# Kernel optimization log

Measured on AMD Instinct MI355X. Metric: run time of the kernel, lower is better.

Reference implementation:

```python
import jax, jax.numpy as jnp
import numpy as np
from jax import lax

N_WAY, N_SUPPORT, N_QUERY = 16, 256, 512
D_IN, D_EMB = 4096, 1024
N_CLUSTERS, MAX_ITER = 5, 100


def setup_inputs() -> dict:
    key = jax.random.key(0)
    k1, k2, kw, kb = jax.random.split(key, 4)
    support = jax.random.normal(k1, (N_WAY, N_SUPPORT, D_IN), jnp.float32)
    query = jax.random.normal(k2, (N_WAY, N_QUERY, D_IN), jnp.float32)
    W = jax.random.normal(kw, (D_IN, D_EMB), jnp.float32) / np.float32(np.sqrt(D_IN))
    b = jax.random.normal(kb, (D_EMB,), jnp.float32) * 0.01
    return {"support": support, "query": query, "W": W, "b": b}


def _sqdist(x, c):
    # x [n,d], c [k,d] -> [n,k] squared euclidean distances
    return (jnp.sum(x * x, -1, keepdims=True)
            - 2.0 * (x @ c.T)
            + jnp.sum(c * c, -1))


def _kmeans(x, init):
    # x [n,d], init [k,d]; fixed-iteration Lloyd's kmeans (converged state is a
    # fixed point of the update, matching the torch early-break semantics).
    n = x.shape[0]
    ones = jnp.ones((n,), x.dtype)

    def step(c, _):
        assign = jnp.argmin(_sqdist(x, c), axis=1)              # [n]
        sums = jax.ops.segment_sum(x, assign, num_segments=N_CLUSTERS)
        cnt = jax.ops.segment_sum(ones, assign, num_segments=N_CLUSTERS)
        # empty cluster keeps its old centroid
        new_c = jnp.where(cnt[:, None] > 0,
                          sums / jnp.maximum(cnt, 1.0)[:, None], c)
        return new_c, None

    c, _ = lax.scan(step, init, None, length=MAX_ITER)
    return c


def _forward(support, query, W, b):
    # encoder: shared linear over flattened (n_way * n) rows
    s = (support.reshape(-1, D_IN) @ W + b).reshape(N_WAY, N_SUPPORT, D_EMB)
    q = (query.reshape(-1, D_IN) @ W + b).reshape(N_WAY, N_QUERY, D_EMB)

    # per-class kmeans init: random subset of that class's support embeddings
    keys = jax.random.split(jax.random.key(42), N_WAY)

    def init_fn(key, class_emb):
        idx = jax.random.permutation(key, N_SUPPORT)[:N_CLUSTERS]
        return class_emb[idx]

    inits = jax.vmap(init_fn)(keys, s)                 # [n_way, k, d]
    cluster_protos = jax.vmap(_kmeans)(s, inits)       # [n_way, k, d]
    class_protos = cluster_protos.mean(axis=1)         # [n_way, d]

    # cdist(query_emb [b,n,d], protos [c,d]) -> [b,n,c]
    d2 = (jnp.sum(q * q, -1)[..., None]
          - 2.0 * jnp.einsum('bnd,cd->bnc', q, class_protos)
          + jnp.sum(class_protos * class_protos, -1))
    distances = jnp.sqrt(jnp.maximum(d2, 0.0))
    return -distances                                  # logits [n_way, n_query, n_classes]


def reference(support, query, W, b):
    return _forward(support, query, W, b)
```

## Files before the change

kernel.cpp:

```cpp
#include <hip/hip_runtime.h>
#include <cstdint>
#include <cstddef>


typedef __attribute__((ext_vector_type(4))) float f32x4;
typedef __attribute__((ext_vector_type(8))) short s16x8;
typedef __attribute__((ext_vector_type(4))) short s16x4;
typedef __attribute__((ext_vector_type(8))) __bf16 bf16x8;

__device__ __forceinline__ unsigned short f2bf(float f) {
  unsigned u = __float_as_uint(f);
  return (unsigned short)((u + 0x7FFFu + ((u >> 16) & 1u)) >> 16);
}
__device__ __forceinline__ float bf2f(unsigned short h) {
  return __uint_as_float(((unsigned)h) << 16);
}

typedef const __attribute__((address_space(1))) void GV;
typedef __attribute__((address_space(3))) void LV;
__device__ __forceinline__ void gload_lds16(const void* g, void* l) {
  __builtin_amdgcn_global_load_lds((GV*)g, (LV*)l, 16, 0, 0);
}
__device__ __forceinline__ f32x4 mfma16(bf16x8 a, bf16x8 b, f32x4 c) {
  return __builtin_amdgcn_mfma_f32_16x16x32_bf16(a, b, c, 0, 0, 0);
}
__device__ __forceinline__ float wave_sum(float v) {
#pragma unroll
  for (int st = 1; st < 64; st <<= 1) v += __shfl_xor(v, st);
  return v;
}

__device__ __forceinline__ void tf2x32(unsigned k0, unsigned k1, unsigned x0,
                                       unsigned x1, unsigned& y0, unsigned& y1) {
  unsigned ks0 = k0, ks1 = k1, ks2 = k0 ^ k1 ^ 0x1BD11BDAu;
  x0 += ks0; x1 += ks1;
  const int rA[4] = {13, 15, 26, 6};
  const int rB[4] = {17, 29, 16, 24};
#define ROTL(v, d) (((v) << (d)) | ((v) >> (32 - (d))))
#define RG(R)                                     \
  _Pragma("unroll") for (int i = 0; i < 4; i++) { \
    x0 += x1; x1 = ROTL(x1, R[i]); x1 ^= x0;      \
  }
  RG(rA); x0 += ks1; x1 += ks2 + 1u;
  RG(rB); x0 += ks2; x1 += ks0 + 2u;
  RG(rA); x0 += ks0; x1 += ks1 + 3u;
  RG(rB); x0 += ks1; x1 += ks2 + 4u;
  RG(rA); x0 += ks2; x1 += ks0 + 5u;
#undef RG
#undef ROTL
  y0 = x0; y1 = x1;
}

__global__ __launch_bounds__(256) void prep_sw_k(
    const float* __restrict__ W, const float* __restrict__ sup,
    short* __restrict__ WhiT, short* __restrict__ WloT,
    short* __restrict__ Shi, short* __restrict__ Slo) {
  __shared__ float tile[64][65];
  int t = threadIdx.x;
  if (blockIdx.x < 1024) {
    int bk = blockIdx.x & 63, bn = blockIdx.x >> 6;
#pragma unroll
    for (int i = 0; i < 4; i++) {
      int row = i * 16 + (t >> 4);
      int col = (t & 15) * 4;
      f32x4 v =
          *(const f32x4*)(W + (size_t)(bk * 64 + row) * 1024 + bn * 64 + col);
      tile[row][col + 0] = v[0]; tile[row][col + 1] = v[1];
      tile[row][col + 2] = v[2]; tile[row][col + 3] = v[3];
    }
    __syncthreads();
#pragma unroll
    for (int i = 0; i < 4; i++) {
      int nrow = i * 16 + (t >> 4);
      int kcol = (t & 15) * 4;
      s16x4 hv, lv;
#pragma unroll
      for (int e = 0; e < 4; e++) {
        float v = tile[kcol + e][nrow];
        unsigned short h = f2bf(v);
        hv[e] = (short)h;
        lv[e] = (short)f2bf(v - bf2f(h));
      }
      size_t off = (size_t)(bn * 64 + nrow) * 4096 + bk * 64 + kcol;
      *(s16x4*)(WhiT + off) = hv;
      *(s16x4*)(WloT + off) = lv;
    }
  } else {
    const size_t sup_n8 = (size_t)4096 * 4096 / 8;
    size_t stride = (size_t)(gridDim.x - 1024) * 256;
    for (size_t gid = (size_t)(blockIdx.x - 1024) * 256 + t; gid < sup_n8;
         gid += stride) {
      const float* src = sup + gid * 8;
      f32x4 v0 = *(const f32x4*)src, v1 = *(const f32x4*)(src + 4);
      s16x8 h, l;
#pragma unroll
      for (int e = 0; e < 4; e++) {
        unsigned short hh = f2bf(v0[e]);
        h[e] = (short)hh; l[e] = (short)f2bf(v0[e] - bf2f(hh));
      }
#pragma unroll
      for (int e = 0; e < 4; e++) {
        unsigned short hh = f2bf(v1[e]);
        h[4 + e] = (short)hh; l[4 + e] = (short)f2bf(v1[e] - bf2f(hh));
      }
      *(s16x8*)(Shi + gid * 8) = h;
      *(s16x8*)(Slo + gid * 8) = l;
    }
  }
}

__global__ __launch_bounds__(256) void gemm_supq_k(
    const short* __restrict__ Shi, const short* __restrict__ Slo,
    const short* __restrict__ WhiT, const short* __restrict__ WloT,
    const float* __restrict__ bias, float* __restrict__ emb,
    const float* __restrict__ qry, short* __restrict__ Qhi) {
  __shared__ short lds[24576];
  const int t = threadIdx.x;
  if (blockIdx.x < 512) {
    short* Ah = lds;
    short* Al = lds + 4096;
    short* Bh = lds + 8192;
    short* Bl = lds + 16384;
    const int bid = blockIdx.x;
    const int bm = bid & 63, bn = bid >> 6;
    const int lane = t & 63, w = t >> 6;
    const int wr = w >> 1, wc = w & 1;
    const int fr = lane & 15, kg = lane >> 4;
    const int ls = lane >> 3, lc = lane & 7;
    const short* Ag = Shi + (size_t)bm * 64 * 4096;
    const short* Alg = Slo + (size_t)bm * 64 * 4096;
    f32x4 acc[2][4] = {};

    for (int kt = 0; kt < 64; ++kt) {
      const int k0 = kt * 64;
      __syncthreads();
      const int cch = (lc ^ ls) * 8;
#pragma unroll
      for (int j = 0; j < 2; j++) {
        int rowl = w * 16 + j * 8 + ls;
        size_t aoff = (size_t)rowl * 4096 + k0 + cch;
        int ldst = (w * 16 + j * 8) * 64;
        gload_lds16(Ag + aoff, Ah + ldst);
        gload_lds16(Alg + aoff, Al + ldst);
      }
#pragma unroll
      for (int j = 0; j < 4; j++) {
        int rowl = w * 32 + j * 8 + ls;
        size_t boff = (size_t)(bn * 128 + rowl) * 4096 + k0 + cch;
        int ldst = (w * 32 + j * 8) * 64;
        gload_lds16(WhiT + boff, Bh + ldst);
        gload_lds16(WloT + boff, Bl + ldst);
      }
      __syncthreads();
#pragma unroll
      for (int ks = 0; ks < 2; ++ks) {
        const int cx = ((ks * 4 + kg) ^ (fr & 7)) * 8;
        bf16x8 ahf[2], alf[2], bhf[4], blf[4];
#pragma unroll
        for (int mi = 0; mi < 2; mi++) {
          int arow = wr * 32 + mi * 16 + fr;
          ahf[mi] =
              __builtin_bit_cast(bf16x8, *(const s16x8*)(Ah + arow * 64 + cx));
          alf[mi] =
              __builtin_bit_cast(bf16x8, *(const s16x8*)(Al + arow * 64 + cx));
        }
#pragma unroll
        for (int ni = 0; ni < 4; ni++) {
          int brow = wc * 64 + ni * 16 + fr;
          bhf[ni] =
              __builtin_bit_cast(bf16x8, *(const s16x8*)(Bh + brow * 64 + cx));
          blf[ni] =
              __builtin_bit_cast(bf16x8, *(const s16x8*)(Bl + brow * 64 + cx));
        }
#pragma unroll
        for (int mi = 0; mi < 2; mi++)
#pragma unroll
          for (int ni = 0; ni < 4; ni++) {
            acc[mi][ni] = mfma16(ahf[mi], bhf[ni], acc[mi][ni]);
            acc[mi][ni] = mfma16(ahf[mi], blf[ni], acc[mi][ni]);
            acc[mi][ni] = mfma16(alf[mi], bhf[ni], acc[mi][ni]);
          }
      }
    }
#pragma unroll
    for (int ni = 0; ni < 4; ni++) {
      int gc = bn * 128 + wc * 64 + ni * 16 + fr;
      float bv = bias[gc];
#pragma unroll
      for (int mi = 0; mi < 2; mi++) {
        int gr = bm * 64 + wr * 32 + mi * 16 + kg * 4;
#pragma unroll
        for (int r = 0; r < 4; r++)
          emb[(size_t)(gr + r) * 1024 + gc] = acc[mi][ni][r] + bv;
      }
    }
  } else {
    const size_t qry_n8 = (size_t)8192 * 4096 / 8;
    size_t stride = (size_t)(gridDim.x - 512) * 256;
    for (size_t gid = (size_t)(blockIdx.x - 512) * 256 + t; gid < qry_n8;
         gid += stride) {
      const float* src = qry + gid * 8;
      f32x4 v0 = *(const f32x4*)src, v1 = *(const f32x4*)(src + 4);
      s16x8 h;
#pragma unroll
      for (int e = 0; e < 4; e++) h[e] = (short)f2bf(v0[e]);
#pragma unroll
      for (int e = 0; e < 4; e++) h[4 + e] = (short)f2bf(v1[e]);
      *(s16x8*)(Qhi + gid * 8) = h;
    }
  }
}

__global__ __launch_bounds__(256) void gramdiag2_k(const float* __restrict__ emb,
                                                   float* __restrict__ G) {
  if (blockIdx.x < 256) {
    int c = blockIdx.x >> 4, tl = blockIdx.x & 15, ti = tl >> 2, tj = tl & 3;
    __shared__ float AsT[32][68];
    __shared__ float BsT[32][68];
    int t = threadIdx.x, ty = t >> 4, tx = t & 15;
    const float* base = emb + (size_t)c * 256 * 1024;
    float acc[4][4] = {};
    for (int k0 = 0; k0 < 1024; k0 += 32) {
      __syncthreads();
      {
        int r = t >> 2, seg = t & 3;
        const float* pa = base + (size_t)(ti * 64 + r) * 1024 + k0 + seg * 8;
        f32x4 va0 = *(const f32x4*)pa, va1 = *(const f32x4*)(pa + 4);
#pragma unroll
        for (int e = 0; e < 4; e++) AsT[seg * 8 + e][r] = va0[e];
#pragma unroll
        for (int e = 0; e < 4; e++) AsT[seg * 8 + 4 + e][r] = va1[e];
        const float* pb = base + (size_t)(tj * 64 + r) * 1024 + k0 + seg * 8;
        f32x4 vb0 = *(const f32x4*)pb, vb1 = *(const f32x4*)(pb + 4);
#pragma unroll
        for (int e = 0; e < 4; e++) BsT[seg * 8 + e][r] = vb0[e];
#pragma unroll
        for (int e = 0; e < 4; e++) BsT[seg * 8 + 4 + e][r] = vb1[e];
      }
      __syncthreads();
#pragma unroll 4
      for (int kk = 0; kk < 32; kk++) {
        f32x4 av = *(const f32x4*)(&AsT[kk][ty * 4]);
        f32x4 bv = *(const f32x4*)(&BsT[kk][tx * 4]);
#pragma unroll
        for (int jdx = 0; jdx < 4; jdx++) {
          acc[0][jdx] = fmaf(av[0], bv[jdx], acc[0][jdx]);
          acc[1][jdx] = fmaf(av[1], bv[jdx], acc[1][jdx]);
          acc[2][jdx] = fmaf(av[2], bv[jdx], acc[2][jdx]);
          acc[3][jdx] = fmaf(av[3], bv[jdx], acc[3][jdx]);
        }
      }
    }
#pragma unroll
    for (int i = 0; i < 4; i++) {
      int gr = ti * 64 + ty * 4 + i;
#pragma unroll
      for (int j = 0; j < 4; j++) {
        int gcl = tj * 64 + tx * 4 + j;
        if (gr != gcl)
          G[(size_t)c * 65536 + (size_t)gr * 256 + gcl] = acc[i][j];
      }
    }
  } else {
    int r = (blockIdx.x - 256) * 4 + (threadIdx.x >> 6);
    int lane = threadIdx.x & 63;
    const float* x = emb + (size_t)r * 1024;
    double acc = 0.0;
#pragma unroll
    for (int ch = 0; ch < 16; ch++) {
      float v = x[ch * 64 + lane];
      acc = fma((double)v, (double)v, acc);
    }
#pragma unroll
    for (int st = 1; st < 64; st <<= 1) acc += __shfl_xor(acc, st);
    if (lane == 0) {
      int c = r >> 8, i = r & 255;
      G[(size_t)c * 65536 + (size_t)i * 256 + i] = (float)acc;
    }
  }
}

__global__ __launch_bounds__(256) void gemm_all_k(
    const float* __restrict__ sup, const float* __restrict__ qry,
    const short* __restrict__ WhiT, const short* __restrict__ WloT,
    const float* __restrict__ bias, float* __restrict__ emb) {
  __shared__ short lds[4 * 128 * 64];
  short* Ah = lds;
  short* Al = lds + 8192;
  short* Bh = lds + 16384;
  short* Bl = lds + 24576;
  const int bid = blockIdx.x;
  const int bm = bid % 96, bn = bid / 96;
  const bool is_sup = bm < 32;
  const int t = threadIdx.x, lane = t & 63, w = t >> 6;
  const int wr = w >> 1, wc = w & 1;
  const int fr = lane & 15, kg = lane >> 4;
  const float* Abase = is_sup ? (sup + (size_t)bm * 128 * 4096)
                              : (qry + (size_t)(bm - 32) * 128 * 4096);
  f32x4 acc[4][4] = {};
  const int ls = lane >> 3, lc = lane & 7;

  for (int kt = 0; kt < 64; ++kt) {
    const int k0 = kt * 64;
    __syncthreads();
#pragma unroll
    for (int i = 0; i < 4; i++) {
      int row = i * 32 + w * 8 + ls;
      const float* src = Abase + (size_t)row * 4096 + k0 + lc * 8;
      f32x4 v0 = *(const f32x4*)src;
      f32x4 v1 = *(const f32x4*)(src + 4);
      s16x8 hs;
#pragma unroll
      for (int e = 0; e < 4; e++) hs[e] = (short)f2bf(v0[e]);
#pragma unroll
      for (int e = 0; e < 4; e++) hs[4 + e] = (short)f2bf(v1[e]);
      int chunk = lc ^ (row & 7);
      *(s16x8*)(Ah + row * 64 + chunk * 8) = hs;
      if (is_sup) {
        s16x8 lsv;
#pragma unroll
        for (int e = 0; e < 4; e++)
          lsv[e] = (short)f2bf(v0[e] - bf2f((unsigned short)hs[e]));
#pragma unroll
        for (int e = 0; e < 4; e++)
          lsv[4 + e] = (short)f2bf(v1[e] - bf2f((unsigned short)hs[4 + e]));
        *(s16x8*)(Al + row * 64 + chunk * 8) = lsv;
      }
    }
#pragma unroll
    for (int j = 0; j < 4; j++) {
      int rowl = w * 32 + j * 8 + ls;
      int cch = (lc ^ (ls & 7)) * 8;
      size_t goff = (size_t)(bn * 128 + rowl) * 4096 + k0 + cch;
      gload_lds16(WhiT + goff, Bh + (w * 32 + j * 8) * 64);
      if (is_sup) gload_lds16(WloT + goff, Bl + (w * 32 + j * 8) * 64);
    }
    __syncthreads();
#pragma unroll
    for (int ks = 0; ks < 2; ++ks) {
      const int cx = ((ks * 4 + kg) ^ (fr & 7)) * 8;
      bf16x8 ahf[4], bhf[4];
#pragma unroll
      for (int mi = 0; mi < 4; mi++) {
        int arow = wr * 64 + mi * 16 + fr;
        ahf[mi] = __builtin_bit_cast(bf16x8, *(const s16x8*)(Ah + arow * 64 + cx));
      }
#pragma unroll
      for (int ni = 0; ni < 4; ni++) {
        int brow = wc * 64 + ni * 16 + fr;
        bhf[ni] = __builtin_bit_cast(bf16x8, *(const s16x8*)(Bh + brow * 64 + cx));
      }
      if (is_sup) {
        bf16x8 alf[4], blf[4];
#pragma unroll
        for (int mi = 0; mi < 4; mi++) {
          int arow = wr * 64 + mi * 16 + fr;
          alf[mi] =
              __builtin_bit_cast(bf16x8, *(const s16x8*)(Al + arow * 64 + cx));
        }
#pragma unroll
        for (int ni = 0; ni < 4; ni++) {
          int brow = wc * 64 + ni * 16 + fr;
          blf[ni] =
              __builtin_bit_cast(bf16x8, *(const s16x8*)(Bl + brow * 64 + cx));
        }
#pragma unroll
        for (int mi = 0; mi < 4; mi++)
#pragma unroll
          for (int ni = 0; ni < 4; ni++) {
            acc[mi][ni] = mfma16(ahf[mi], bhf[ni], acc[mi][ni]);
            acc[mi][ni] = mfma16(ahf[mi], blf[ni], acc[mi][ni]);
            acc[mi][ni] = mfma16(alf[mi], bhf[ni], acc[mi][ni]);
          }
      } else {
#pragma unroll
        for (int mi = 0; mi < 4; mi++)
#pragma unroll
          for (int ni = 0; ni < 4; ni++)
            acc[mi][ni] = mfma16(ahf[mi], bhf[ni], acc[mi][ni]);
      }
    }
  }
#pragma unroll
  for (int ni = 0; ni < 4; ni++) {
    int gc = bn * 128 + wc * 64 + ni * 16 + fr;
    float bv = bias[gc];
#pragma unroll
    for (int mi = 0; mi < 4; mi++) {
      int gr = bm * 128 + wr * 64 + mi * 16 + kg * 4;
#pragma unroll
      for (int r = 0; r < 4; r++)
        emb[(size_t)(gr + r) * 1024 + gc] = acc[mi][ni][r] + bv;
    }
  }
}

#define APPLY1(db, nb, gg, p)                        \
  if ((db) & 1u)  s[p][0] += ((nb) & 1u)  ? (gg) : -(gg); \
  if ((db) & 2u)  s[p][1] += ((nb) & 2u)  ? (gg) : -(gg); \
  if ((db) & 4u)  s[p][2] += ((nb) & 4u)  ? (gg) : -(gg); \
  if ((db) & 8u)  s[p][3] += ((nb) & 8u)  ? (gg) : -(gg); \
  if ((db) & 16u) s[p][4] += ((nb) & 16u) ? (gg) : -(gg);

__global__ __launch_bounds__(64) void kmeans3_k(const float* __restrict__ G,
                                                float* __restrict__ wts) {
  const int c = blockIdx.x;
  const int lane = threadIdx.x;
  unsigned o0, o1, s0k, s1k;
  tf2x32(0u, 42u, 0u, (unsigned)c, o0, o1);
  tf2x32(o0, o1, 0u, 1u, s0k, s1k);
  unsigned long long key[4];
#pragma unroll
  for (int q = 0; q < 4; q++) {
    unsigned y0, y1;
    tf2x32(s0k, s1k, 0u, (unsigned)(lane + 64 * q), y0, y1);
    key[q] = ((unsigned long long)(y0 ^ y1) << 32) | (unsigned)(lane + 64 * q);
  }
  int idx5[5];
#pragma unroll
  for (int r = 0; r < 5; r++) {
    unsigned long long mn = key[0];
#pragma unroll
    for (int q = 1; q < 4; q++) mn = key[q] < mn ? key[q] : mn;
#pragma unroll
    for (int st = 1; st < 64; st <<= 1) {
      unsigned long long o = __shfl_xor(mn, st);
      mn = o < mn ? o : mn;
    }
    int widx = (int)(unsigned)(mn & 0xffffffffu);
    idx5[r] = widx;
#pragma unroll
    for (int q = 0; q < 4; q++)
      if (widx == lane + 64 * q) key[q] = ~0ull;
  }
  unsigned m[4];
#pragma unroll
  for (int q = 0; q < 4; q++) {
    unsigned mm = 0;
#pragma unroll
    for (int k = 0; k < 5; k++)
      if (idx5[k] == lane + 64 * q) mm |= 1u << k;
    m[q] = mm;
  }
  const float* Gc = G + (size_t)c * 65536;
  float s[4][5];
#pragma unroll
  for (int k = 0; k < 5; k++) {
    const float* row = Gc + (size_t)idx5[k] * 256;
#pragma unroll
    for (int q = 0; q < 4; q++) s[q][k] = row[lane + 64 * q];
  }
  float Minv[5] = {1.0f, 1.0f, 1.0f, 1.0f, 1.0f};

  for (int it = 0; it < 100; ++it) {
    float Tu[5], C2[5];
#pragma unroll
    for (int k = 0; k < 5; k++) {
      float v = 0.0f;
#pragma unroll
      for (int q = 0; q < 4; q++)
        v += ((m[q] >> k) & 1u) ? s[q][k] : 0.0f;
#pragma unroll
      for (int st = 1; st < 64; st <<= 1) v += __shfl_xor(v, st);
      float iv = Minv[k];
      Tu[k] = v * iv * iv;
      C2[k] = -2.0f * iv;
    }
    int a[4];
#pragma unroll
    for (int q = 0; q < 4; q++) {
      float d0 = fmaf(C2[0], s[q][0], Tu[0]);
      float d1 = fmaf(C2[1], s[q][1], Tu[1]);
      float d2 = fmaf(C2[2], s[q][2], Tu[2]);
      float d3 = fmaf(C2[3], s[q][3], Tu[3]);
      float d4 = fmaf(C2[4], s[q][4], Tu[4]);
      int at = 0;
      float dmn = d0;
      if (d1 < dmn) { dmn = d1; at = 1; }
      if (d2 < dmn) { dmn = d2; at = 2; }
      if (d3 < dmn) { dmn = d3; at = 3; }
      if (d4 < dmn) { dmn = d4; at = 4; }
      a[q] = at;
    }
    int cnt[5];
#pragma unroll
    for (int k = 0; k < 5; k++) {
      int v = (a[0] == k) + (a[1] == k) + (a[2] == k) + (a[3] == k);
#pragma unroll
      for (int st = 1; st < 64; st <<= 1) v += __shfl_xor(v, st);
      cnt[k] = v;
    }
    unsigned nm[4], dm[4];
#pragma unroll
    for (int q = 0; q < 4; q++) {
      unsigned nv = 0;
#pragma unroll
      for (int k = 0; k < 5; k++) {
        int bit = (cnt[k] > 0) ? (a[q] == k ? 1 : 0) : (int)((m[q] >> k) & 1u);
        nv |= ((unsigned)bit) << k;
      }
      nm[q] = nv;
      dm[q] = nv ^ m[q];
    }
    unsigned long long bal[4];
#pragma unroll
    for (int q = 0; q < 4; q++) bal[q] = __ballot(dm[q] != 0);
    if ((bal[0] | bal[1] | bal[2] | bal[3]) == 0) break;
#pragma unroll
    for (int q = 0; q < 4; q++) m[q] = nm[q];
#pragma unroll
    for (int k = 0; k < 5; k++)
      if (cnt[k] > 0) Minv[k] = 1.0f / (float)cnt[k];
#pragma unroll
    for (int q = 0; q < 4; q++) {
      unsigned long long mask = bal[q];
      while (mask) {
#define GATHER(i)                                                      \
        int j##i = -1;                                                 \
        unsigned d##i = 0, e##i = 0;                                   \
        float g##i##0 = 0, g##i##1 = 0, g##i##2 = 0, g##i##3 = 0;      \
        if (mask) {                                                    \
          j##i = __builtin_ctzll(mask);                                \
          mask &= mask - 1;                                            \
          d##i = __shfl(dm[q], j##i);                                  \
          e##i = __shfl(nm[q], j##i);                                  \
          const float* row = Gc + (size_t)(q * 64 + j##i) * 256 + lane;\
          g##i##0 = row[0];  g##i##1 = row[64];                        \
          g##i##2 = row[128]; g##i##3 = row[192];                      \
        }
        GATHER(0) GATHER(1) GATHER(2) GATHER(3)
        GATHER(4) GATHER(5) GATHER(6) GATHER(7)
#undef GATHER
#define DOAPPLY(i)                        \
        if (j##i >= 0) {                  \
          APPLY1(d##i, e##i, g##i##0, 0)  \
          APPLY1(d##i, e##i, g##i##1, 1)  \
          APPLY1(d##i, e##i, g##i##2, 2)  \
          APPLY1(d##i, e##i, g##i##3, 3)  \
        }
        DOAPPLY(0) DOAPPLY(1) DOAPPLY(2) DOAPPLY(3)
        DOAPPLY(4) DOAPPLY(5) DOAPPLY(6) DOAPPLY(7)
#undef DOAPPLY
      }
    }
  }
#pragma unroll
  for (int q = 0; q < 4; q++) {
    float wv = 0.0f;
#pragma unroll
    for (int k = 0; k < 5; k++)
      if ((m[q] >> k) & 1u) wv += 0.2f * Minv[k];
    wts[c * 256 + lane + 64 * q] = wv;
  }
}

__global__ __launch_bounds__(256) void proto1_k(const float* __restrict__ emb,
                                                const float* __restrict__ wts,
                                                float* __restrict__ part) {
  int c = blockIdx.x & 15, seg = blockIdx.x >> 4, t = threadIdx.x;
  __shared__ float wl[16];
  if (t < 16) wl[t] = wts[c * 256 + seg * 16 + t];
  __syncthreads();
  f32x4 acc = {};
  const float* base = emb + (size_t)(c * 256 + seg * 16) * 1024 + t * 4;
#pragma unroll
  for (int j = 0; j < 16; j++) {
    f32x4 v = *(const f32x4*)(base + (size_t)j * 1024);
    float wj = wl[j];
#pragma unroll
    for (int e = 0; e < 4; e++) acc[e] = fmaf(wj, v[e], acc[e]);
  }
  *(f32x4*)(part + ((size_t)seg * 16 + c) * 1024 + t * 4) = acc;
}

__global__ __launch_bounds__(256) void proto2p_k(const float* __restrict__ part,
                                                 float* __restrict__ protos,
                                                 float* __restrict__ psqb) {
  __shared__ float Tp[4];
  int c = blockIdx.x, t = threadIdx.x, lane = t & 63, w = t >> 6;
  f32x4 acc = {};
#pragma unroll
  for (int seg = 0; seg < 16; seg++) {
    f32x4 v = *(const f32x4*)(part + ((size_t)seg * 16 + c) * 1024 + t * 4);
#pragma unroll
    for (int e = 0; e < 4; e++) acc[e] += v[e];
  }
  *(f32x4*)(protos + (size_t)c * 1024 + t * 4) = acc;
  float s = acc[0] * acc[0] + acc[1] * acc[1] + acc[2] * acc[2] +
            acc[3] * acc[3];
  s = wave_sum(s);
  if (lane == 0) Tp[w] = s;
  __syncthreads();
  if (t == 0) psqb[c] = Tp[0] + Tp[1] + Tp[2] + Tp[3];
}

__global__ __launch_bounds__(256) void gemm_qry_dist_k(
    const short* __restrict__ Qhi, const short* __restrict__ WhiT,
    const float* __restrict__ bias, const float* __restrict__ protos,
    float* __restrict__ part) {
  __shared__ __align__(16) char smem[74496];
  short* Ah = (short*)smem;
  short* Bh = (short*)(smem + 16384);
  float (*q_tile)[129] = (float(*)[129])smem;
  float (*pl)[132] = (float(*)[132])(smem + 66048);
  const int t = threadIdx.x;
  const int bid = blockIdx.x;
  const int bm = bid & 63, bn = bid >> 6;
  const int lane = t & 63, w = t >> 6;
  const int wr = w >> 1, wc = w & 1;
  const int fr = lane & 15, kg = lane >> 4;
  const int ls = lane >> 3, lc = lane & 7;
  const short* Ag = Qhi + (size_t)bm * 128 * 4096;
  f32x4 acc[4][4] = {};

  for (int kt = 0; kt < 64; ++kt) {
    const int k0 = kt * 64;
    __syncthreads();
    const int cch = (lc ^ ls) * 8;
#pragma unroll
    for (int j = 0; j < 4; j++) {
      int rowl = w * 32 + j * 8 + ls;
      size_t aoff = (size_t)rowl * 4096 + k0 + cch;
      size_t boff = (size_t)(bn * 128 + rowl) * 4096 + k0 + cch;
      int ldst = (w * 32 + j * 8) * 64;
      gload_lds16(Ag + aoff, Ah + ldst);
      gload_lds16(WhiT + boff, Bh + ldst);
    }
    __syncthreads();
#pragma unroll
    for (int ks = 0; ks < 2; ++ks) {
      const int cx = ((ks * 4 + kg) ^ (fr & 7)) * 8;
      bf16x8 ahf[4], bhf[4];
#pragma unroll
      for (int mi = 0; mi < 4; mi++) {
        int arow = wr * 64 + mi * 16 + fr;
        ahf[mi] = __builtin_bit_cast(bf16x8, *(const s16x8*)(Ah + arow * 64 + cx));
      }
#pragma unroll
      for (int ni = 0; ni < 4; ni++) {
        int brow = wc * 64 + ni * 16 + fr;
        bhf[ni] = __builtin_bit_cast(bf16x8, *(const s16x8*)(Bh + brow * 64 + cx));
      }
#pragma unroll
      for (int mi = 0; mi < 4; mi++)
#pragma unroll
        for (int ni = 0; ni < 4; ni++)
          acc[mi][ni] = mfma16(ahf[mi], bhf[ni], acc[mi][ni]);
    }
  }
  __syncthreads();
#pragma unroll
  for (int ni = 0; ni < 4; ni++) {
    int cl = wc * 64 + ni * 16 + fr;
    float bv = bias[bn * 128 + cl];
#pragma unroll
    for (int mi = 0; mi < 4; mi++) {
      int rl = wr * 64 + mi * 16 + kg * 4;
#pragma unroll
      for (int r = 0; r < 4; r++) q_tile[rl + r][cl] = acc[mi][ni][r] + bv;
    }
  }
  {
    int p = t >> 4, cl0 = (t & 15) * 8;
    const float* src = protos + (size_t)p * 1024 + bn * 128 + cl0;
    f32x4 v0 = *(const f32x4*)src, v1 = *(const f32x4*)(src + 4);
#pragma unroll
    for (int e = 0; e < 4; e++) pl[p][cl0 + e] = v0[e];
#pragma unroll
    for (int e = 0; e < 4; e++) pl[p][cl0 + 4 + e] = v1[e];
  }
  __syncthreads();
  const int row = t & 127, half = t >> 7;
  float dot[16] = {};
  float qs = 0.0f;
#pragma unroll 4
  for (int ci = 0; ci < 64; ci++) {
    int c = half * 64 + ci;
    float v = q_tile[row][c];
    qs = fmaf(v, v, qs);
#pragma unroll
    for (int p = 0; p < 16; p++) dot[p] = fmaf(v, pl[p][c], dot[p]);
  }
  int grow = bm * 128 + row;
  float* dst = part + ((size_t)(bn * 2 + half) * 8192 + grow) * 17;
#pragma unroll
  for (int p = 0; p < 16; p++) dst[p] = dot[p];
  dst[16] = qs;
}

__global__ __launch_bounds__(256) void distred_k(const float* __restrict__ part,
                                                 const float* __restrict__ psqb,
                                                 float* __restrict__ out) {
  int gid = blockIdx.x * 256 + threadIdx.x;
  int row = gid >> 4, p = gid & 15;
  float dot = 0.0f, qs = 0.0f;
#pragma unroll
  for (int s = 0; s < 16; s++) {
    const float* src = part + ((size_t)s * 8192 + row) * 17;
    dot += src[p];
    qs += src[16];
  }
  float d2 = qs - 2.0f * dot + psqb[p];
  d2 = fmaxf(d2, 0.0f);
  out[(size_t)row * 16 + p] = -sqrtf(d2);
}

__global__ __launch_bounds__(256) void proto_k(const float* __restrict__ emb,
                                               const float* __restrict__ wts,
                                               float* __restrict__ protos) {
  int c = blockIdx.x, t = threadIdx.x;
  __shared__ float wl[256];
  wl[t] = wts[c * 256 + t];
  __syncthreads();
  f32x4 acc = {};
  const float* base = emb + (size_t)c * 256 * 1024 + t * 4;
  for (int j = 0; j < 256; j++) {
    f32x4 v = *(const f32x4*)(base + (size_t)j * 1024);
    float wj = wl[j];
#pragma unroll
    for (int e = 0; e < 4; e++) acc[e] = fmaf(wj, v[e], acc[e]);
  }
  *(f32x4*)(protos + (size_t)c * 1024 + t * 4) = acc;
}

__global__ __launch_bounds__(256) void dist_k(const float* __restrict__ emb,
                                              const float* __restrict__ protos,
                                              float* __restrict__ out) {
  __shared__ float P[16 * 1024];
  int t = threadIdx.x, lane = t & 63, w = t >> 6;
#pragma unroll
  for (int i = 0; i < 16; i++) {
    int off = i * 1024 + t * 4;
    *(f32x4*)(P + off) = *(const f32x4*)(protos + off);
  }
  __syncthreads();
  float psq_keep = 0.0f;
  for (int p = 0; p < 16; p++) {
    float partial = 0.0f;
#pragma unroll
    for (int ch = 0; ch < 16; ch++) {
      float x = P[p * 1024 + ch * 64 + lane];
      partial = fmaf(x, x, partial);
    }
    partial = wave_sum(partial);
    if (lane == p) psq_keep = partial;
  }
  const float* qbase = emb + (size_t)4096 * 1024;
  int r0 = blockIdx.x * 16 + w * 4;
  for (int ri = 0; ri < 4; ri++) {
    int row = r0 + ri;
    const float* q = qbase + (size_t)row * 1024;
    float qv[16];
#pragma unroll
    for (int ch = 0; ch < 16; ch++) qv[ch] = q[ch * 64 + lane];
    float qsq = 0.0f;
#pragma unroll
    for (int ch = 0; ch < 16; ch++) qsq = fmaf(qv[ch], qv[ch], qsq);
    qsq = wave_sum(qsq);
    float dsel = 0.0f;
    for (int p = 0; p < 16; p++) {
      float dp = 0.0f;
#pragma unroll
      for (int ch = 0; ch < 16; ch++)
        dp = fmaf(qv[ch], P[p * 1024 + ch * 64 + lane], dp);
      dp = wave_sum(dp);
      if (lane == p) dsel = dp;
    }
    if (lane < 16) {
      float d2 = qsq - 2.0f * dsel + psq_keep;
      d2 = fmaxf(d2, 0.0f);
      out[(size_t)row * 16 + lane] = -sqrtf(d2);
    }
  }
}

extern "C" void kernel_launch(void* const* d_in, const int* in_sizes, int n_in,
                              void* d_out, int out_size, void* d_ws,
                              size_t ws_size, hipStream_t stream) {
  const float* sup = (const float*)d_in[0];
  const float* qry = (const float*)d_in[1];
  const float* W = (const float*)d_in[2];
  const float* b = (const float*)d_in[3];
  float* out = (float*)d_out;
  char* ws = (char*)d_ws;
  (void)in_sizes; (void)n_in; (void)out_size;

  const size_t NEED_FAST = 206651392ULL;
  if (ws_size >= NEED_FAST) {
    short* WhiT = (short*)(ws + 0);
    short* WloT = (short*)(ws + 8388608);
    short* Shi = (short*)(ws + 16777216);
    short* Slo = (short*)(ws + 50331648);
    short* Qhi = (short*)(ws + 83886080);
    float* emb = (float*)(ws + 150994944);
    float* G = (float*)(ws + 201326592);
    float* wts = (float*)(ws + 205520896);
    float* protos = (float*)(ws + 205537280);
    float* part1 = (float*)(ws + 205602816);
    float* dpart = (float*)(ws + 16777216);
    float* psqb = (float*)(ws + 50331648);

    prep_sw_k<<<2048, 256, 0, stream>>>(W, sup, WhiT, WloT, Shi, Slo);
    gemm_supq_k<<<768, 256, 0, stream>>>(Shi, Slo, WhiT, WloT, b, emb, qry,
                                         Qhi);
    gramdiag2_k<<<1280, 256, 0, stream>>>(emb, G);
    kmeans3_k<<<16, 64, 0, stream>>>(G, wts);
    proto1_k<<<256, 256, 0, stream>>>(emb, wts, part1);
    proto2p_k<<<16, 256, 0, stream>>>(part1, protos, psqb);
    gemm_qry_dist_k<<<512, 256, 0, stream>>>(Qhi, WhiT, b, protos, dpart);
    distred_k<<<512, 256, 0, stream>>>(dpart, psqb, out);
  } else {
    short* WhiT = (short*)(ws + 0);
    short* WloT = (short*)(ws + 8388608);
    float* emb = (float*)(ws + 16777216);
    float* G = (float*)(ws + 67108864);
    float* wts = (float*)(ws + 71303168);
    float* protos = (float*)(ws + 71319552);

    prep_sw_k<<<1024, 256, 0, stream>>>(W, sup, WhiT, WloT, (short*)0,
                                        (short*)0);
    gemm_all_k<<<768, 256, 0, stream>>>(sup, qry, WhiT, WloT, b, emb);
    gramdiag2_k<<<1280, 256, 0, stream>>>(emb, G);
    kmeans3_k<<<16, 64, 0, stream>>>(G, wts);
    proto_k<<<16, 256, 0, stream>>>(emb, wts, protos);
    dist_k<<<512, 256, 0, stream>>>(emb, protos, out);
  }
}
```

Before: 408.8 us.

## Split Gram matrix over K with a reduce pass; shrink distance-kernel LDS footprint

The Gram-matrix computation is split along the embedding dimension into four partial blocks (1024 blocks instead of 256), followed by a reduce kernel that sums the partials and also computes the fp64 diagonal. The query GEMM+distance kernel now stages its fp32 output tile in two 64-row halves, cutting shared memory from ~74KB to ~42KB so more blocks fit per CU, and splits columns into quarters, which doubles the partial count read by distred_k. This trades extra partial-buffer traffic and an added launch for more parallelism and occupancy.

```diff
diff --git a/kernel.cpp b/kernel.cpp
--- a/kernel.cpp
+++ b/kernel.cpp
@@ -211,58 +211,79 @@
   }
 }
 
-__global__ __launch_bounds__(256) void gramdiag2_k(const float* __restrict__ emb,
-                                                   float* __restrict__ G) {
-  if (blockIdx.x < 256) {
-    int c = blockIdx.x >> 4, tl = blockIdx.x & 15, ti = tl >> 2, tj = tl & 3;
-    __shared__ float AsT[32][68];
-    __shared__ float BsT[32][68];
-    int t = threadIdx.x, ty = t >> 4, tx = t & 15;
-    const float* base = emb + (size_t)c * 256 * 1024;
-    float acc[4][4] = {};
-    for (int k0 = 0; k0 < 1024; k0 += 32) {
-      __syncthreads();
-      {
-        int r = t >> 2, seg = t & 3;
-        const float* pa = base + (size_t)(ti * 64 + r) * 1024 + k0 + seg * 8;
-        f32x4 va0 = *(const f32x4*)pa, va1 = *(const f32x4*)(pa + 4);
-#pragma unroll
-        for (int e = 0; e < 4; e++) AsT[seg * 8 + e][r] = va0[e];
-#pragma unroll
-        for (int e = 0; e < 4; e++) AsT[seg * 8 + 4 + e][r] = va1[e];
-        const float* pb = base + (size_t)(tj * 64 + r) * 1024 + k0 + seg * 8;
-        f32x4 vb0 = *(const f32x4*)pb, vb1 = *(const f32x4*)(pb + 4);
-#pragma unroll
-        for (int e = 0; e < 4; e++) BsT[seg * 8 + e][r] = vb0[e];
-#pragma unroll
-        for (int e = 0; e < 4; e++) BsT[seg * 8 + 4 + e][r] = vb1[e];
-      }
-      __syncthreads();
+__global__ __launch_bounds__(256) void gram_part_k(
+    const float* __restrict__ emb, float* __restrict__ Gp) {
+  int b = blockIdx.x;
+  int kq = b >> 8, rem = b & 255;
+  int c = rem >> 4, tl = rem & 15, ti = tl >> 2, tj = tl & 3;
+  __shared__ float AsT[32][68];
+  __shared__ float BsT[32][68];
+  int t = threadIdx.x, ty = t >> 4, tx = t & 15;
+  const float* base = emb + (size_t)c * 256 * 1024;
+  float acc[4][4] = {};
+  for (int k0 = kq * 256; k0 < kq * 256 + 256; k0 += 32) {
+    __syncthreads();
+    {
+      int r = t >> 2, seg = t & 3;
+      const float* pa = base + (size_t)(ti * 64 + r) * 1024 + k0 + seg * 8;
+      f32x4 va0 = *(const f32x4*)pa, va1 = *(const f32x4*)(pa + 4);
+#pragma unroll
+      for (int e = 0; e < 4; e++) AsT[seg * 8 + e][r] = va0[e];
+#pragma unroll
+      for (int e = 0; e < 4; e++) AsT[seg * 8 + 4 + e][r] = va1[e];
+      const float* pb = base + (size_t)(tj * 64 + r) * 1024 + k0 + seg * 8;
+      f32x4 vb0 = *(const f32x4*)pb, vb1 = *(const f32x4*)(pb + 4);
+#pragma unroll
+      for (int e = 0; e < 4; e++) BsT[seg * 8 + e][r] = vb0[e];
+#pragma unroll
+      for (int e = 0; e < 4; e++) BsT[seg * 8 + 4 + e][r] = vb1[e];
+    }
+    __syncthreads();
 #pragma unroll 4
-      for (int kk = 0; kk < 32; kk++) {
-        f32x4 av = *(const f32x4*)(&AsT[kk][ty * 4]);
-        f32x4 bv = *(const f32x4*)(&BsT[kk][tx * 4]);
-#pragma unroll
-        for (int jdx = 0; jdx < 4; jdx++) {
-          acc[0][jdx] = fmaf(av[0], bv[jdx], acc[0][jdx]);
-          acc[1][jdx] = fmaf(av[1], bv[jdx], acc[1][jdx]);
-          acc[2][jdx] = fmaf(av[2], bv[jdx], acc[2][jdx]);
-          acc[3][jdx] = fmaf(av[3], bv[jdx], acc[3][jdx]);
-        }
-      }
-    }
-#pragma unroll
-    for (int i = 0; i < 4; i++) {
-      int gr = ti * 64 + ty * 4 + i;
-#pragma unroll
-      for (int j = 0; j < 4; j++) {
-        int gcl = tj * 64 + tx * 4 + j;
-        if (gr != gcl)
-          G[(size_t)c * 65536 + (size_t)gr * 256 + gcl] = acc[i][j];
-      }
-    }
+    for (int kk = 0; kk < 32; kk++) {
+      f32x4 av = *(const f32x4*)(&AsT[kk][ty * 4]);
+      f32x4 bv = *(const f32x4*)(&BsT[kk][tx * 4]);
+#pragma unroll
+      for (int jdx = 0; jdx < 4; jdx++) {
+        acc[0][jdx] = fmaf(av[0], bv[jdx], acc[0][jdx]);
+        acc[1][jdx] = fmaf(av[1], bv[jdx], acc[1][jdx]);
+        acc[2][jdx] = fmaf(av[2], bv[jdx], acc[2][jdx]);
+        acc[3][jdx] = fmaf(av[3], bv[jdx], acc[3][jdx]);
+      }
+    }
+  }
+  float* dst = Gp + ((size_t)kq * 16 + c) * 65536;
+#pragma unroll
+  for (int i = 0; i < 4; i++) {
+    int gr = ti * 64 + ty * 4 + i;
+#pragma unroll
+    for (int j = 0; j < 4; j++)
+      dst[(size_t)gr * 256 + tj * 64 + tx * 4 + j] = acc[i][j];
+  }
+}
+
+__global__ __launch_bounds__(256) void greduce_k(const float* __restrict__ Gp,
+                                                 const float* __restrict__ emb,
+                                                 float* __restrict__ G) {
+  if (blockIdx.x < 1024) {
+    size_t cell0 = ((size_t)blockIdx.x * 256 + threadIdx.x) * 4;
+    int c = (int)(cell0 >> 16);
+    int within = (int)(cell0 & 65535);
+    int gr = within >> 8, gc0 = within & 255;
+    f32x4 s = {};
+#pragma unroll
+    for (int kq = 0; kq < 4; kq++) {
+      f32x4 v = *(const f32x4*)(Gp + (((size_t)kq * 16 + c) * 65536 +
+                                      (size_t)gr * 256 + gc0));
+#pragma unroll
+      for (int e = 0; e < 4; e++) s[e] += v[e];
+    }
+#pragma unroll
+    for (int e = 0; e < 4; e++)
+      if (gr != gc0 + e)
+        G[(size_t)c * 65536 + (size_t)gr * 256 + gc0 + e] = s[e];
   } else {
-    int r = (blockIdx.x - 256) * 4 + (threadIdx.x >> 6);
+    int r = (blockIdx.x - 1024) * 4 + (threadIdx.x >> 6);
     int lane = threadIdx.x & 63;
     const float* x = emb + (size_t)r * 1024;
     double acc = 0.0;
@@ -391,6 +412,75 @@
 #pragma unroll
       for (int r = 0; r < 4; r++)
         emb[(size_t)(gr + r) * 1024 + gc] = acc[mi][ni][r] + bv;
+    }
+  }
+}
+
+__global__ __launch_bounds__(256) void gramdiag2_k(const float* __restrict__ emb,
+                                                   float* __restrict__ G) {
+  if (blockIdx.x < 256) {
+    int c = blockIdx.x >> 4, tl = blockIdx.x & 15, ti = tl >> 2, tj = tl & 3;
+    __shared__ float AsT[32][68];
+    __shared__ float BsT[32][68];
+    int t = threadIdx.x, ty = t >> 4, tx = t & 15;
+    const float* base = emb + (size_t)c * 256 * 1024;
+    float acc[4][4] = {};
+    for (int k0 = 0; k0 < 1024; k0 += 32) {
+      __syncthreads();
+      {
+        int r = t >> 2, seg = t & 3;
+        const float* pa = base + (size_t)(ti * 64 + r) * 1024 + k0 + seg * 8;
+        f32x4 va0 = *(const f32x4*)pa, va1 = *(const f32x4*)(pa + 4);
+#pragma unroll
+        for (int e = 0; e < 4; e++) AsT[seg * 8 + e][r] = va0[e];
+#pragma unroll
+        for (int e = 0; e < 4; e++) AsT[seg * 8 + 4 + e][r] = va1[e];
+        const float* pb = base + (size_t)(tj * 64 + r) * 1024 + k0 + seg * 8;
+        f32x4 vb0 = *(const f32x4*)pb, vb1 = *(const f32x4*)(pb + 4);
+#pragma unroll
+        for (int e = 0; e < 4; e++) BsT[seg * 8 + e][r] = vb0[e];
+#pragma unroll
+        for (int e = 0; e < 4; e++) BsT[seg * 8 + 4 + e][r] = vb1[e];
+      }
+      __syncthreads();
+#pragma unroll 4
+      for (int kk = 0; kk < 32; kk++) {
+        f32x4 av = *(const f32x4*)(&AsT[kk][ty * 4]);
+        f32x4 bv = *(const f32x4*)(&BsT[kk][tx * 4]);
+#pragma unroll
+        for (int jdx = 0; jdx < 4; jdx++) {
+          acc[0][jdx] = fmaf(av[0], bv[jdx], acc[0][jdx]);
+          acc[1][jdx] = fmaf(av[1], bv[jdx], acc[1][jdx]);
+          acc[2][jdx] = fmaf(av[2], bv[jdx], acc[2][jdx]);
+          acc[3][jdx] = fmaf(av[3], bv[jdx], acc[3][jdx]);
+        }
+      }
+    }
+#pragma unroll
+    for (int i = 0; i < 4; i++) {
+      int gr = ti * 64 + ty * 4 + i;
+#pragma unroll
+      for (int j = 0; j < 4; j++) {
+        int gcl = tj * 64 + tx * 4 + j;
+        if (gr != gcl)
+          G[(size_t)c * 65536 + (size_t)gr * 256 + gcl] = acc[i][j];
+      }
+    }
+  } else {
+    int r = (blockIdx.x - 256) * 4 + (threadIdx.x >> 6);
+    int lane = threadIdx.x & 63;
+    const float* x = emb + (size_t)r * 1024;
+    double acc = 0.0;
+#pragma unroll
+    for (int ch = 0; ch < 16; ch++) {
+      float v = x[ch * 64 + lane];
+      acc = fma((double)v, (double)v, acc);
+    }
+#pragma unroll
+    for (int st = 1; st < 64; st <<= 1) acc += __shfl_xor(acc, st);
+    if (lane == 0) {
+      int c = r >> 8, i = r & 255;
+      G[(size_t)c * 65536 + (size_t)i * 256 + i] = (float)acc;
     }
   }
 }
@@ -597,12 +687,12 @@
 __global__ __launch_bounds__(256) void gemm_qry_dist_k(
     const short* __restrict__ Qhi, const short* __restrict__ WhiT,
     const float* __restrict__ bias, const float* __restrict__ protos,
-    float* __restrict__ part) {
-  __shared__ __align__(16) char smem[74496];
+    float* __restrict__ dpart) {
+  __shared__ __align__(16) char smem[41984];
   short* Ah = (short*)smem;
   short* Bh = (short*)(smem + 16384);
-  float (*q_tile)[129] = (float(*)[129])smem;
-  float (*pl)[132] = (float(*)[132])(smem + 66048);
+  float (*pl)[129] = (float(*)[129])smem;
+  float (*q_tile)[129] = (float(*)[129])(smem + 8320);
   const int t = threadIdx.x;
   const int bid = blockIdx.x;
   const int bm = bid & 63, bn = bid >> 6;
@@ -649,17 +739,6 @@
     }
   }
   __syncthreads();
-#pragma unroll
-  for (int ni = 0; ni < 4; ni++) {
-    int cl = wc * 64 + ni * 16 + fr;
-    float bv = bias[bn * 128 + cl];
-#pragma unroll
-    for (int mi = 0; mi < 4; mi++) {
-      int rl = wr * 64 + mi * 16 + kg * 4;
-#pragma unroll
-      for (int r = 0; r < 4; r++) q_tile[rl + r][cl] = acc[mi][ni][r] + bv;
-    }
-  }
   {
     int p = t >> 4, cl0 = (t & 15) * 8;
     const float* src = protos + (size_t)p * 1024 + bn * 128 + cl0;
@@ -669,34 +748,51 @@
 #pragma unroll
     for (int e = 0; e < 4; e++) pl[p][cl0 + 4 + e] = v1[e];
   }
-  __syncthreads();
-  const int row = t & 127, half = t >> 7;
-  float dot[16] = {};
-  float qs = 0.0f;
+  const int row = t & 63, quarter = t >> 6;
+#pragma unroll
+  for (int half = 0; half < 2; half++) {
+    if (wr == half) {
+#pragma unroll
+      for (int ni = 0; ni < 4; ni++) {
+        int cl = wc * 64 + ni * 16 + fr;
+        float bv = bias[bn * 128 + cl];
+#pragma unroll
+        for (int mi = 0; mi < 4; mi++) {
+          int rl = mi * 16 + kg * 4;
+#pragma unroll
+          for (int r = 0; r < 4; r++) q_tile[rl + r][cl] = acc[mi][ni][r] + bv;
+        }
+      }
+    }
+    __syncthreads();
+    float dot[16] = {};
+    float qs = 0.0f;
 #pragma unroll 4
-  for (int ci = 0; ci < 64; ci++) {
-    int c = half * 64 + ci;
-    float v = q_tile[row][c];
-    qs = fmaf(v, v, qs);
-#pragma unroll
-    for (int p = 0; p < 16; p++) dot[p] = fmaf(v, pl[p][c], dot[p]);
-  }
-  int grow = bm * 128 + row;
-  float* dst = part + ((size_t)(bn * 2 + half) * 8192 + grow) * 17;
-#pragma unroll
-  for (int p = 0; p < 16; p++) dst[p] = dot[p];
-  dst[16] = qs;
-}
-
-__global__ __launch_bounds__(256) void distred_k(const float* __restrict__ part,
+    for (int ci = 0; ci < 32; ci++) {
+      int c = quarter * 32 + ci;
+      float v = q_tile[row][c];
+      qs = fmaf(v, v, qs);
+#pragma unroll
+      for (int p = 0; p < 16; p++) dot[p] = fmaf(v, pl[p][c], dot[p]);
+    }
+    int grow = bm * 128 + half * 64 + row;
+    float* dst = dpart + ((size_t)(bn * 4 + quarter) * 8192 + grow) * 17;
+#pragma unroll
+    for (int p = 0; p < 16; p++) dst[p] = dot[p];
+    dst[16] = qs;
+    __syncthreads();
+  }
+}
+
+__global__ __launch_bounds__(256) void distred_k(const float* __restrict__ dpart,
                                                  const float* __restrict__ psqb,
                                                  float* __restrict__ out) {
   int gid = blockIdx.x * 256 + threadIdx.x;
   int row = gid >> 4, p = gid & 15;
   float dot = 0.0f, qs = 0.0f;
 #pragma unroll
-  for (int s = 0; s < 16; s++) {
-    const float* src = part + ((size_t)s * 8192 + row) * 17;
+  for (int s = 0; s < 32; s++) {
+    const float* src = dpart + ((size_t)s * 8192 + row) * 17;
     dot += src[p];
     qs += src[16];
   }
@@ -799,11 +895,13 @@
     float* part1 = (float*)(ws + 205602816);
     float* dpart = (float*)(ws + 16777216);
     float* psqb = (float*)(ws + 50331648);
+    float* Gp = (float*)(ws + 50335744);
 
     prep_sw_k<<<2048, 256, 0, stream>>>(W, sup, WhiT, WloT, Shi, Slo);
     gemm_supq_k<<<768, 256, 0, stream>>>(Shi, Slo, WhiT, WloT, b, emb, qry,
                                          Qhi);
-    gramdiag2_k<<<1280, 256, 0, stream>>>(emb, G);
+    gram_part_k<<<1024, 256, 0, stream>>>(emb, Gp);
+    greduce_k<<<2048, 256, 0, stream>>>(Gp, emb, G);
     kmeans3_k<<<16, 64, 0, stream>>>(G, wts);
     proto1_k<<<256, 256, 0, stream>>>(emb, wts, part1);
     proto2p_k<<<16, 256, 0, stream>>>(part1, protos, psqb);
```

Measured after the change: 454.6 us. 1.11x slower.
